# Kernel tuning notes

Hardware: AMD Instinct MI355X
Metric: run time of the kernel (lower is better)

Reference implementation:

```python
import jax, jax.numpy as jnp
import numpy as np

B, T, D, H = 4, 2048, 1024, 4
DK = D // H      # head_k_dim = 256
DV = D // H      # head_v_dim = 256
M = DK           # num_slots defaults to head_k_dim
GATE_NORM = 16.0
CLAMP_MIN, CLAMP_MAX = -32.0, 32.0
EPS = 1e-5
ROPE_BASE = 10000.0


def setup_inputs() -> dict:
    key = jax.random.key(0)
    ks = jax.random.split(key, 8)
    sd = 0.02  # stands in for xavier_uniform with gain 2**-2.5
    return {
        "hidden_states": jax.random.normal(ks[0], (B, T, D), jnp.float32),
        "q_w": jax.random.normal(ks[1], (D, D), jnp.float32) * sd,
        "k_w": jax.random.normal(ks[2], (D, D), jnp.float32) * sd,
        "v_w": jax.random.normal(ks[3], (D, D), jnp.float32) * sd,
        "g_w": jax.random.normal(ks[4], (D, D), jnp.float32) * sd,
        "s_w": jax.random.normal(ks[5], (D, H * M), jnp.float32) * sd,
        "sg_w": jax.random.normal(ks[6], (D, H), jnp.float32) * sd,
        "gn_w": jnp.ones((DV,), jnp.float32),
        "o_w": jax.random.normal(ks[7], (D, D), jnp.float32) * sd,
    }


def _rope(x):
    # x: [B, T, H, DK]; non-interleaved (flash-attn style) rotary, full head dim
    half = x.shape[-1] // 2
    inv = 1.0 / (ROPE_BASE ** (jnp.arange(half, dtype=jnp.float32) / half))
    ang = jnp.arange(x.shape[1], dtype=jnp.float32)[:, None] * inv[None, :]  # [T, half]
    cos = jnp.cos(ang)[None, :, None, :]
    sin = jnp.sin(ang)[None, :, None, :]
    x1, x2 = x[..., :half], x[..., half:]
    return jnp.concatenate([x1 * cos - x2 * sin, x2 * cos + x1 * sin], -1)


def _abc(q, k, v, s):
    # ABC linear attention with slot memory (fla chunk_abc semantics, g=None path).
    # q, k: [B,H,T,DK]; v: [B,H,T,DV]; s: [B,H,T,M] (clamped slot logits)
    scale = q.shape[-1] ** -0.5
    z = jax.lax.cumlogsumexp(s, axis=2)                    # running log-normalizer
    s_n = jnp.exp(s - z)                                   # normalized slot write weights
    g = jnp.exp(jnp.concatenate([z[:, :, :1], z[:, :, :-1]], 2) - z)  # per-step decay in (0,1]

    tm = lambda x: jnp.moveaxis(x, 2, 0)                   # time-major for scan

    # stage 1: key memory  hk[B,H,DK,M];  ok_t = scale * q_t @ hk_t
    def step_k(hk, inp):
        q_t, k_t, s_t, g_t = inp
        hk = hk * g_t[:, :, None, :] + k_t[..., None] * s_t[:, :, None, :]
        return hk, jnp.einsum('bhk,bhkm->bhm', q_t, hk)
    hk0 = jnp.zeros(q.shape[:2] + (q.shape[-1], s.shape[-1]), q.dtype)
    _, ok = jax.lax.scan(step_k, hk0, (tm(q * scale), tm(k), tm(s_n), tm(g)))

    qv = jax.nn.softmax(ok, axis=-1)                       # slot read weights, [T,B,H,M]

    # stage 2: value memory  hv[B,H,M,DV];  ov_t = qv_t @ hv_t
    def step_v(hv, inp):
        qv_t, v_t, s_t, g_t = inp
        hv = hv * g_t[..., None] + s_t[..., None] * v_t[:, :, None, :]
        return hv, jnp.einsum('bhm,bhmv->bhv', qv_t, hv)
    hv0 = jnp.zeros(v.shape[:2] + (s.shape[-1], v.shape[-1]), v.dtype)
    _, ov = jax.lax.scan(step_v, hv0, (qv, tm(v), tm(s_n), tm(g)))
    return jnp.moveaxis(ov, 0, 2)                          # [B,H,T,DV]


def reference(hidden_states, q_w, k_w, v_w, g_w, s_w, sg_w, gn_w, o_w):
    x = hidden_states
    q = (x @ q_w).reshape(B, T, H, DK)
    k = (x @ k_w).reshape(B, T, H, DK)
    v = (x @ v_w).reshape(B, T, H, DV).transpose(0, 2, 1, 3)       # [B,H,T,DV]
    q, k = _rope(q), _rope(k)
    q = q.transpose(0, 2, 1, 3)                                    # [B,H,T,DK]
    k = k.transpose(0, 2, 1, 3)

    s = (x @ s_w).reshape(B, T, H, M).transpose(0, 2, 1, 3)        # [B,H,T,M]
    s = jnp.clip(s, CLAMP_MIN, CLAMP_MAX)

    sg = jax.nn.log_sigmoid(x @ sg_w).transpose(0, 2, 1) / GATE_NORM  # [B,H,T]
    k = k * jnp.exp(jnp.cumsum(sg, axis=2))[..., None]

    o = _abc(q, k, v, s).transpose(0, 2, 1, 3)                     # [B,T,H,DV]

    g = (x @ g_w).reshape(B, T, H, DV)
    rms = o * jax.lax.rsqrt(jnp.mean(o * o, axis=-1, keepdims=True) + EPS) * gn_w
    o = (rms * g * jax.nn.sigmoid(g)).reshape(B, T, D)             # RMSNorm + swish gate
    return o @ o_w
```

## Files before the change

kernel.cpp:

```cpp
#include <hip/hip_runtime.h>
#include <hip/hip_bf16.h>
#include <stdint.h>
#include <stddef.h>
#include <math.h>

typedef __bf16 bf8_t __attribute__((ext_vector_type(8)));
typedef float  f4_t  __attribute__((ext_vector_type(4)));
typedef unsigned int u32;

#define DEV static __device__ __forceinline__

namespace abc {
constexpr int B = 4, T = 2048, D = 1024, H = 4;
constexpr int BT = B * T;
constexpr int CH = 64;
constexpr int NC = T / CH;
constexpr int BH = B * H;
constexpr float SCALE = 0.0625f;
constexpr float GN = 16.0f;
constexpr float EPS = 1e-5f;
}

DEV f4_t mfma16(bf8_t a, bf8_t b, f4_t c) {
  return __builtin_amdgcn_mfma_f32_16x16x32_bf16(a, b, c, 0, 0, 0);
}

DEV void glds16(const void* g, void* l) {
  __builtin_amdgcn_global_load_lds(
      (const __attribute__((address_space(1))) u32*)g,
      (__attribute__((address_space(3))) u32*)l, 16, 0, 0);
}

DEV __bf16* slice_addr(__bf16* base, int row, int cg ) {
  return base + (((cg >> 2) * 2 + (row >> 7)) * 4096
               + ((((row & 127) << 2) | ((cg & 3) ^ (row & 3))) * 8));
}
DEV const __bf16* slice_addr(const __bf16* base, int row, int cg) {
  return base + (((cg >> 2) * 2 + (row >> 7)) * 4096
               + ((((row & 127) << 2) | ((cg & 3) ^ (row & 3))) * 8));
}

DEV void stage_g(const __bf16* __restrict__ g, int S, __bf16* lds, int tid) {
  int m = tid >> 2;
  int q = (tid & 3) ^ ((m >> 1) & 3);
  glds16(g + (size_t)m * S + q * 8, lds + (tid & ~63) * 8);
}
DEV bf8_t bfrag_g(const __bf16* sl, int m, int quad) {
  return *reinterpret_cast<const bf8_t*>(sl + m * 32 + (((quad ^ (m >> 1)) & 3) << 3));
}

__global__ __launch_bounds__(256)
void cvt_x_kernel(const float* __restrict__ x, __bf16* __restrict__ xb)
{
  const int idx = blockIdx.x * 256 + threadIdx.x;
  const float4* src = reinterpret_cast<const float4*>(x);
  float4 a = src[(size_t)idx * 2];
  float4 b = src[(size_t)idx * 2 + 1];
  bf8_t o;
  o[0] = (__bf16)a.x; o[1] = (__bf16)a.y; o[2] = (__bf16)a.z; o[3] = (__bf16)a.w;
  o[4] = (__bf16)b.x; o[5] = (__bf16)b.y; o[6] = (__bf16)b.z; o[7] = (__bf16)b.w;
  reinterpret_cast<bf8_t*>(xb)[idx] = o;
}

__global__ __launch_bounds__(256)
void cvt_w_kernel(const float* __restrict__ w0, const float* __restrict__ w1,
                  const float* __restrict__ w2, const float* __restrict__ w3,
                  const float* __restrict__ w4, const float* __restrict__ w5,
                  __bf16* __restrict__ wt)
{
  const int z = blockIdx.z;
  const float* W = (z == 0) ? w0 : (z == 1) ? w1 : (z == 2) ? w2
                 : (z == 3) ? w3 : (z == 4) ? w4 : w5;
  const int n0 = blockIdx.x * 64, k0 = blockIdx.y * 64;
  __shared__ __bf16 Ts[64][72];
  const int tid = threadIdx.x;
  #pragma unroll
  for (int i = 0; i < 4; i++) {
    int p = tid + 256 * i;
    int row = p >> 4, c4 = p & 15;
    float4 v = *reinterpret_cast<const float4*>(W + (size_t)(k0 + row) * 1024 + n0 + c4 * 4);
    Ts[c4 * 4 + 0][row] = (__bf16)v.x;
    Ts[c4 * 4 + 1][row] = (__bf16)v.y;
    Ts[c4 * 4 + 2][row] = (__bf16)v.z;
    Ts[c4 * 4 + 3][row] = (__bf16)v.w;
  }
  __syncthreads();
  #pragma unroll
  for (int i = 0; i < 2; i++) {
    int p = tid + 256 * i;
    int n = p >> 3, kq = p & 7;
    bf8_t o = *reinterpret_cast<const bf8_t*>(&Ts[n][kq * 8]);
    *reinterpret_cast<bf8_t*>(wt + (size_t)z * 1024 * 1024 + (size_t)(n0 + n) * 1024 + k0 + kq * 8) = o;
  }
}

template<bool OUT_BF16, int NZ>
__global__ __launch_bounds__(512, 2)
void gemm256_kernel(const __bf16* __restrict__ A, const __bf16* __restrict__ BtB,
                    void* __restrict__ Cp)
{
  using namespace abc;
  constexpr int K = 1024;
  constexpr int NZT = 4 * NZ;
  const int bflat = blockIdx.x;
  const int xcd = bflat & 7;
  const int j = bflat >> 3;
  const int m_local = j / NZT;
  const int nz = j % NZT;
  const int nt = nz & 3, z = nz >> 2;
  const int m0 = (xcd * 4 + m_local) * 256;
  const int n0 = nt * 256;
  const __bf16* Bt = BtB + (size_t)z * K * 1024;

  __shared__ __bf16 LA[2][4][4096];
  __shared__ __bf16 LB[2][4][4096];

  const int tid = threadIdx.x;
  const int lane = tid & 63, wv = tid >> 6;
  const int wr = wv >> 2, wc = wv & 3;
  const int quad = lane >> 4, l16 = lane & 15;
  const f4_t fzero = {0.f, 0.f, 0.f, 0.f};
  f4_t acc[8][4];
  #pragma unroll
  for (int fr = 0; fr < 8; fr++)
    #pragma unroll
    for (int fc = 0; fc < 4; fc++) acc[fr][fc] = fzero;

  auto issue4 = [&](int kt, int ks) {
    const int db = kt & 1;
    const int kcol = kt * 64 + ks * 32;
    stage_g(A  + (size_t)(m0 +   0) * K + kcol, K, &LA[db][0 + ks][0], tid);
    stage_g(A  + (size_t)(m0 + 128) * K + kcol, K, &LA[db][2 + ks][0], tid);
    stage_g(Bt + (size_t)(n0 +   0) * K + kcol, K, &LB[db][0 + ks][0], tid);
    stage_g(Bt + (size_t)(n0 + 128) * K + kcol, K, &LB[db][2 + ks][0], tid);
  };

  issue4(0, 0); issue4(0, 1);

  for (int kt = 0; kt < 16; kt++) {
    const int db = kt & 1;
    const bool last = (kt == 15);
    #pragma unroll
    for (int ks = 0; ks < 2; ks++) {
      if (last && ks == 1) asm volatile("s_waitcnt vmcnt(0)\ns_barrier" ::: "memory");
      else                 asm volatile("s_waitcnt vmcnt(4)\ns_barrier" ::: "memory");
      bf8_t af[8], bfv[4];
      #pragma unroll
      for (int fr = 0; fr < 8; fr++)
        af[fr] = bfrag_g(&LA[db][wr * 2 + ks][0], fr * 16 + l16, quad);
      #pragma unroll
      for (int fc = 0; fc < 4; fc++)
        bfv[fc] = bfrag_g(&LB[db][(wc >> 1) * 2 + ks][0], (wc & 1) * 64 + fc * 16 + l16, quad);
      if (!last) issue4(kt + 1, ks);
      __builtin_amdgcn_s_setprio(1);
      #pragma unroll
      for (int fr = 0; fr < 8; fr++)
        #pragma unroll
        for (int fc = 0; fc < 4; fc++)
          acc[fr][fc] = mfma16(af[fr], bfv[fc], acc[fr][fc]);
      __builtin_amdgcn_s_setprio(0);
    }
  }

  const int crow = m0 + wr * 128, ccol = n0 + wc * 64;
  if (OUT_BF16) {
    __bf16* C = (__bf16*)Cp + (size_t)z * BT * 1024;
    #pragma unroll
    for (int fr = 0; fr < 8; fr++)
      #pragma unroll
      for (int fc = 0; fc < 4; fc++)
        #pragma unroll
        for (int r = 0; r < 4; r++)
          C[(size_t)(crow + fr * 16 + quad * 4 + r) * 1024 + ccol + fc * 16 + l16] =
              (__bf16)acc[fr][fc][r];
  } else {
    float* C = (float*)Cp;
    #pragma unroll
    for (int fr = 0; fr < 8; fr++)
      #pragma unroll
      for (int fc = 0; fc < 4; fc++)
        #pragma unroll
        for (int r = 0; r < 4; r++)
          C[(size_t)(crow + fr * 16 + quad * 4 + r) * 1024 + ccol + fc * 16 + l16] =
              acc[fr][fc][r];
  }
}

__global__ __launch_bounds__(256)
void sg_kernel(const float* __restrict__ x, const float* __restrict__ sgw,
               float* __restrict__ sgl)
{
  using namespace abc;
  const int wvid = threadIdx.x >> 6, lane = threadIdx.x & 63;
  const int bt = blockIdx.x * 4 + wvid;
  const float* xr = x + (size_t)bt * 1024;
  float a0 = 0, a1 = 0, a2 = 0, a3 = 0;
  #pragma unroll 4
  for (int u = 0; u < 16; u++) {
    int i = u * 64 + lane;
    float xv = xr[i];
    float4 w = *reinterpret_cast<const float4*>(sgw + (size_t)i * 4);
    a0 += xv * w.x; a1 += xv * w.y; a2 += xv * w.z; a3 += xv * w.w;
  }
  #pragma unroll
  for (int off = 32; off > 0; off >>= 1) {
    a0 += __shfl_down(a0, off);
    a1 += __shfl_down(a1, off);
    a2 += __shfl_down(a2, off);
    a3 += __shfl_down(a3, off);
  }
  if (lane == 0) {
    const int b = bt >> 11, t = bt & (T - 1);
    float r[4] = {a0, a1, a2, a3};
    #pragma unroll
    for (int h = 0; h < 4; h++) {
      float v = r[h];
      float ls = fminf(v, 0.f) - log1pf(expf(-fabsf(v)));
      sgl[(size_t)(b * 4 + h) * T + t] = ls * (1.0f / GN);
    }
  }
}

__global__ __launch_bounds__(256)
void scan_kernel(const float* __restrict__ sgl, float* __restrict__ sgc)
{
  using namespace abc;
  const int bh = blockIdx.x;
  const float* in = sgl + (size_t)bh * T;
  float* out = sgc + (size_t)bh * T;
  __shared__ float part[256];
  const int tid = threadIdx.x;
  float v[8]; float s = 0.f;
  #pragma unroll
  for (int i = 0; i < 8; i++) { v[i] = in[tid * 8 + i]; s += v[i]; }
  part[tid] = s;
  __syncthreads();
  for (int off = 1; off < 256; off <<= 1) {
    float a = (tid >= off) ? part[tid - off] : 0.f;
    __syncthreads();
    part[tid] += a;
    __syncthreads();
  }
  float run = (tid > 0) ? part[tid - 1] : 0.f;
  #pragma unroll
  for (int i = 0; i < 8; i++) { run += v[i]; out[tid * 8 + i] = run; }
}

__global__ __launch_bounds__(256)
void prep_kernel(__bf16* __restrict__ q, __bf16* __restrict__ k,
                 __bf16* __restrict__ s, const float* __restrict__ sgc)
{
  using namespace abc;
  const int bt = blockIdx.x;
  const int b = bt >> 11, t = bt & (T - 1);
  const int tid = threadIdx.x;
  const size_t ro = (size_t)bt * 1024;
  #pragma unroll
  for (int i = 0; i < 2; i++) {
    int p = tid + 256 * i;
    int h = p >> 7, d = p & 127;
    float inv = expf(-(float)d * (9.210340371976184f / 128.0f));
    float ang = (float)t * inv;
    float sn, cs;
    sincosf(ang, &sn, &cs);
    size_t base = ro + (size_t)h * 256 + d;
    float q1 = (float)q[base], q2 = (float)q[base + 128];
    q[base]       = (__bf16)(q1 * cs - q2 * sn);
    q[base + 128] = (__bf16)(q2 * cs + q1 * sn);
    float dec = expf(sgc[(size_t)(b * 4 + h) * T + t]);
    float k1 = (float)k[base], k2 = (float)k[base + 128];
    k[base]       = (__bf16)((k1 * cs - k2 * sn) * dec);
    k[base + 128] = (__bf16)((k2 * cs + k1 * sn) * dec);
  }
  #pragma unroll
  for (int i = 0; i < 4; i++) {
    int e = tid + 256 * i;
    float v = (float)s[ro + e];
    v = fminf(fmaxf(v, -32.f), 32.f);
    s[ro + e] = (__bf16)expf(v);
  }
}

template<bool NEW0, bool NEW1>
__global__ __launch_bounds__(256)
void transpose_kernel(const __bf16* __restrict__ s0, const __bf16* __restrict__ s1,
                      __bf16* __restrict__ d0, __bf16* __restrict__ d1)
{
  using namespace abc;
  const int c = blockIdx.x, bh = blockIdx.y, z = blockIdx.z;
  const int b = bh >> 2, h = bh & 3;
  const size_t R = (size_t)b * T + (size_t)c * CH;
  const int F = h * 256;
  const __bf16* src = z ? s1 : s0;
  __bf16* dst = (z ? d1 : d0) + ((size_t)bh * NC + c) * (256 * 64);
  const bool NEWL = z ? NEW1 : NEW0;
  __shared__ __bf16 L[256 * 64];
  const int tid = threadIdx.x;
  #pragma unroll
  for (int j = 0; j < 8; j++) {
    int p = tid + 256 * j;
    int t = p >> 5, fc = p & 31;
    bf8_t v = *reinterpret_cast<const bf8_t*>(src + (R + t) * 1024 + F + fc * 8);
    const int sw = ((t >> 3) ^ (fc & 7)) * 8 + (t & 7);
    #pragma unroll
    for (int u = 0; u < 8; u++)
      L[(fc * 8 + u) * 64 + sw] = v[u];
  }
  __syncthreads();
  #pragma unroll
  for (int j = 0; j < 8; j++) {
    int p = tid + 256 * j;
    int f = p >> 3, q = p & 7;
    int phys = q ^ ((f >> 3) & 7);
    bf8_t o = *reinterpret_cast<const bf8_t*>(&L[f * 64 + phys * 8]);
    __bf16* daddr = NEWL ? slice_addr(dst, f, q)
                         : dst + (size_t)f * 64 + q * 8;
    *reinterpret_cast<bf8_t*>(daddr) = o;
  }
}

__global__ __launch_bounds__(256)
void chunkstate_kernel(const __bf16* __restrict__ KT, const __bf16* __restrict__ VT,
                       const __bf16* __restrict__ AT,
                       __bf16* __restrict__ HKc, __bf16* __restrict__ HVc,
                       float* __restrict__ csA)
{
  using namespace abc;
  const int c = blockIdx.x, bh = blockIdx.y, part = blockIdx.z;
  const size_t TB = ((size_t)bh * NC + c) * (256 * 64);
  const bool isHV = part >= 2;
  const int p2 = part & 1;
  const __bf16* Aop = (isHV ? VT : AT) + TB;
  const __bf16* Bop = (isHV ? AT : KT) + TB;
  const int tid = threadIdx.x;
  if (part == 2) {
    float ssum = 0.f;
    #pragma unroll
    for (int u = 0; u < 8; u++) {
      bf8_t v = *reinterpret_cast<const bf8_t*>(slice_addr(AT + TB, tid, u));
      #pragma unroll
      for (int w = 0; w < 8; w++) ssum += (float)v[w];
    }
    csA[((size_t)bh * NC + c) * 256 + tid] = ssum;
  }
  const int lane = tid & 63, wvid = tid >> 6;
  const int quad = lane >> 4, l16 = lane & 15;
  const int row0 = p2 * 128 + wvid * 32;
  const f4_t fzero = {0.f, 0.f, 0.f, 0.f};
  f4_t acc[2][16];
  #pragma unroll
  for (int a = 0; a < 2; a++)
    #pragma unroll
    for (int ct = 0; ct < 16; ct++) acc[a][ct] = fzero;
  #pragma unroll
  for (int ks = 0; ks < 2; ks++) {
    const int cg = ks * 4 + quad;
    bf8_t af0 = *reinterpret_cast<const bf8_t*>(slice_addr(Aop, row0 + l16, cg));
    bf8_t af1 = *reinterpret_cast<const bf8_t*>(slice_addr(Aop, row0 + 16 + l16, cg));
    #pragma unroll
    for (int ct = 0; ct < 16; ct++) {
      bf8_t bv;
      if (isHV)
        bv = *reinterpret_cast<const bf8_t*>(slice_addr(Bop, ct * 16 + l16, cg));
      else
        bv = *reinterpret_cast<const bf8_t*>(Bop + (size_t)(ct * 16 + l16) * 64 + ks * 32 + quad * 8);
      acc[0][ct] = mfma16(af0, bv, acc[0][ct]);
      acc[1][ct] = mfma16(af1, bv, acc[1][ct]);
    }
  }
  __bf16* out = (isHV ? HVc : HKc) + ((size_t)bh * NC + c) * 65536;
  #pragma unroll
  for (int rt = 0; rt < 2; rt++)
    #pragma unroll
    for (int ct = 0; ct < 16; ct++)
      #pragma unroll
      for (int r = 0; r < 4; r++) {
        const int mg = row0 + rt * 16 + quad * 4 + r;
        const int n  = ct * 16 + l16;
        *(slice_addr(out, mg, n >> 3) + (n & 7)) = (__bf16)acc[rt][ct][r];
      }
}

__global__ __launch_bounds__(256)
void prefix_state_kernel(__bf16* __restrict__ HKc, __bf16* __restrict__ HVc)
{
  using namespace abc;
  const int bh = blockIdx.y;
  __bf16* base = (blockIdx.z ? HVc : HKc) + (size_t)bh * NC * 65536;
  const int e = (blockIdx.x * 256 + threadIdx.x) * 8;
  float run[8];
  #pragma unroll
  for (int u = 0; u < 8; u++) run[u] = 0.f;
  #pragma unroll 4
  for (int c = 0; c < NC; c++) {
    __bf16* p = base + (size_t)c * 65536 + e;
    bf8_t v = *reinterpret_cast<const bf8_t*>(p);
    bf8_t o;
    #pragma unroll
    for (int u = 0; u < 8; u++) { o[u] = (__bf16)run[u]; run[u] += (float)v[u]; }
    *reinterpret_cast<bf8_t*>(p) = o;
  }
}

__global__ __launch_bounds__(256)
void prefix_csa_kernel(float* __restrict__ csA)
{
  using namespace abc;
  const int bh = blockIdx.x, m = threadIdx.x;
  float run = 0.f;
  for (int c = 0; c < NC; c++) {
    float* p = csA + ((size_t)bh * NC + c) * 256 + m;
    float v = *p; *p = run; run += v;
  }
}

__global__ __launch_bounds__(256)
void attn_kernel(const __bf16* __restrict__ qg, const __bf16* __restrict__ kg,
                 const __bf16* __restrict__ ag, const __bf16* __restrict__ gg,
                 const __bf16* __restrict__ ATp, const __bf16* __restrict__ VTp,
                 const __bf16* __restrict__ HKp, const __bf16* __restrict__ HVp,
                 const float* __restrict__ Zp, const float* __restrict__ gnw,
                 __bf16* __restrict__ yout)
{
  using namespace abc;
  const int c = blockIdx.x, bh = blockIdx.y;
  const int b = bh >> 2, h = bh & 3;
  const size_t R = (size_t)b * T + (size_t)c * CH;
  const int F = h * 256;
  const int tid = threadIdx.x;
  const int lane = tid & 63, wvid = tid >> 6;
  const int quad = lane >> 4, l16 = lane & 15;

  __shared__ __bf16 Ws[64][264];
  __shared__ __bf16 S1s[64][72];
  __shared__ float zs[256];
  __shared__ float gns[256];

  const __bf16* atb = ATp + ((size_t)bh * NC + c) * (256 * 64);
  const __bf16* vtb = VTp + ((size_t)bh * NC + c) * (256 * 64);
  const __bf16* hkb = HKp + ((size_t)bh * NC + c) * 65536;
  const __bf16* hvb = HVp + ((size_t)bh * NC + c) * 65536;
  const __bf16* kbase = kg + R * 1024 + F;
  const __bf16* abase = ag + R * 1024 + F;

  zs[tid] = Zp[((size_t)bh * NC + c) * 256 + tid];
  gns[tid] = gnw[tid];
  __syncthreads();

  const int lsw = l16 * 32 + ((quad ^ (l16 & 3)) << 3);
  const int rowoff = l16 * 1024 + quad * 8;

  const __bf16* qrow = qg + (R + wvid * 16 + l16) * 1024 + F;
  bf8_t aq[8];
  #pragma unroll
  for (int ks = 0; ks < 8; ks++)
    aq[ks] = *reinterpret_cast<const bf8_t*>(qrow + ks * 32 + quad * 8);

  const f4_t fzero = {0.f, 0.f, 0.f, 0.f};

  f4_t s1a[4];
  #pragma unroll
  for (int it = 0; it < 4; it++) s1a[it] = fzero;
  #pragma unroll
  for (int ks = 0; ks < 8; ks++) {
    #pragma unroll
    for (int it = 0; it < 4; it++) {
      bf8_t bk = *reinterpret_cast<const bf8_t*>(kbase + it * 16 * 1024 + rowoff + ks * 32);
      s1a[it] = mfma16(aq[ks], bk, s1a[it]);
    }
  }
  #pragma unroll
  for (int it = 0; it < 4; it++)
    #pragma unroll
    for (int r = 0; r < 4; r++) {
      int tl = wvid * 16 + quad * 4 + r;
      int il = it * 16 + l16;
      S1s[tl][il] = (il <= tl) ? (__bf16)s1a[it][r] : (__bf16)0.0f;
    }

  f4_t aok[16], acum[16];
  #pragma unroll
  for (int mt = 0; mt < 16; mt++) { aok[mt] = fzero; acum[mt] = fzero; }
  #pragma unroll
  for (int iks = 0; iks < 2; iks++) {
    bf8_t s1f = *reinterpret_cast<const bf8_t*>(&S1s[wvid * 16 + l16][iks * 32 + quad * 8]);
    bf8_t lf;
    #pragma unroll
    for (int u = 0; u < 8; u++)
      lf[u] = (iks * 32 + quad * 8 + u <= wvid * 16 + l16) ? (__bf16)1.0f : (__bf16)0.0f;
    #pragma unroll
    for (int rh = 0; rh < 2; rh++) {
      #pragma unroll
      for (int m8 = 0; m8 < 8; m8++) {
        bf8_t bfa = *reinterpret_cast<const bf8_t*>(atb + (iks * 2 + rh) * 4096 + m8 * 512 + lsw);
        aok[rh * 8 + m8]  = mfma16(s1f, bfa, aok[rh * 8 + m8]);
        acum[rh * 8 + m8] = mfma16(lf,  bfa, acum[rh * 8 + m8]);
      }
    }
  }

  #pragma unroll
  for (int ks = 0; ks < 8; ks++) {
    #pragma unroll
    for (int rh = 0; rh < 2; rh++) {
      #pragma unroll
      for (int m8 = 0; m8 < 8; m8++) {
        bf8_t bv = *reinterpret_cast<const bf8_t*>(hkb + (ks * 2 + rh) * 4096 + m8 * 512 + lsw);
        aok[rh * 8 + m8] = mfma16(aq[ks], bv, aok[rh * 8 + m8]);
      }
    }
  }

  #pragma unroll
  for (int r = 0; r < 4; r++) {
    float ovv[16], sa[16];
    float mx = -3.0e38f;
    #pragma unroll
    for (int mt = 0; mt < 16; mt++) {
      sa[mt] = zs[mt * 16 + l16] + acum[mt][r];
      ovv[mt] = SCALE * aok[mt][r] / sa[mt];
      mx = fmaxf(mx, ovv[mt]);
    }
    #pragma unroll
    for (int off = 1; off < 16; off <<= 1) mx = fmaxf(mx, __shfl_xor(mx, off));
    float se = 0.f;
    #pragma unroll
    for (int mt = 0; mt < 16; mt++) { ovv[mt] = __expf(ovv[mt] - mx); se += ovv[mt]; }
    #pragma unroll
    for (int off = 1; off < 16; off <<= 1) se += __shfl_xor(se, off);
    float inv = 1.0f / se;
    int tl = wvid * 16 + quad * 4 + r;
    #pragma unroll
    for (int mt = 0; mt < 16; mt++)
      Ws[tl][mt * 16 + l16] = (__bf16)(ovv[mt] * inv / sa[mt]);
  }

  f4_t pacc[4];
  #pragma unroll
  for (int it = 0; it < 4; it++) pacc[it] = fzero;
  #pragma unroll
  for (int ks = 0; ks < 8; ks++) {
    bf8_t wf = *reinterpret_cast<const bf8_t*>(&Ws[wvid * 16 + l16][ks * 32 + quad * 8]);
    #pragma unroll
    for (int it = 0; it < 4; it++) {
      bf8_t ba = *reinterpret_cast<const bf8_t*>(abase + it * 16 * 1024 + rowoff + ks * 32);
      pacc[it] = mfma16(wf, ba, pacc[it]);
    }
  }
  #pragma unroll
  for (int it = 0; it < 4; it++)
    #pragma unroll
    for (int r = 0; r < 4; r++) {
      int tl = wvid * 16 + quad * 4 + r;
      int il = it * 16 + l16;
      S1s[tl][il] = (il <= tl) ? (__bf16)pacc[it][r] : (__bf16)0.0f;
    }

  f4_t oacc[16];
  #pragma unroll
  for (int vt = 0; vt < 16; vt++) oacc[vt] = fzero;
  #pragma unroll
  for (int ks = 0; ks < 8; ks++) {
    bf8_t wf = *reinterpret_cast<const bf8_t*>(&Ws[wvid * 16 + l16][ks * 32 + quad * 8]);
    #pragma unroll
    for (int rh = 0; rh < 2; rh++) {
      #pragma unroll
      for (int v8 = 0; v8 < 8; v8++) {
        bf8_t bv = *reinterpret_cast<const bf8_t*>(hvb + (ks * 2 + rh) * 4096 + v8 * 512 + lsw);
        oacc[rh * 8 + v8] = mfma16(wf, bv, oacc[rh * 8 + v8]);
      }
    }
  }

  #pragma unroll
  for (int iks = 0; iks < 2; iks++) {
    bf8_t pf = *reinterpret_cast<const bf8_t*>(&S1s[wvid * 16 + l16][iks * 32 + quad * 8]);
    #pragma unroll
    for (int rh = 0; rh < 2; rh++) {
      #pragma unroll
      for (int v8 = 0; v8 < 8; v8++) {
        bf8_t bvt = *reinterpret_cast<const bf8_t*>(vtb + (iks * 2 + rh) * 4096 + v8 * 512 + lsw);
        oacc[rh * 8 + v8] = mfma16(pf, bvt, oacc[rh * 8 + v8]);
      }
    }
  }

  #pragma unroll
  for (int r = 0; r < 4; r++) {
    float ss = 0.f;
    #pragma unroll
    for (int vt = 0; vt < 16; vt++) ss += oacc[vt][r] * oacc[vt][r];
    #pragma unroll
    for (int off = 1; off < 16; off <<= 1) ss += __shfl_xor(ss, off);
    float rinv = rsqrtf(ss * (1.0f / 256.0f) + EPS);
    int tl = wvid * 16 + quad * 4 + r;
    const __bf16* grow = gg + (R + tl) * 1024 + F;
    __bf16* yrow = yout + (R + tl) * 1024 + F;
    #pragma unroll
    for (int vt = 0; vt < 16; vt++) {
      int v = vt * 16 + l16;
      float gvl = (float)grow[v];
      float yv = oacc[vt][r] * rinv * gns[v] * gvl / (1.0f + __expf(-gvl));
      yrow[v] = (__bf16)yv;
    }
  }
}

extern "C" void kernel_launch(void* const* d_in, const int* in_sizes, int n_in,
                              void* d_out, int out_size, void* d_ws, size_t ws_size,
                              hipStream_t stream) {
  using namespace abc;
  (void)in_sizes; (void)n_in; (void)out_size; (void)ws_size;
  const float* x    = (const float*)d_in[0];
  const float* q_w  = (const float*)d_in[1];
  const float* k_w  = (const float*)d_in[2];
  const float* v_w  = (const float*)d_in[3];
  const float* g_w  = (const float*)d_in[4];
  const float* s_w  = (const float*)d_in[5];
  const float* sg_w = (const float*)d_in[6];
  const float* gn_w = (const float*)d_in[7];
  const float* o_w  = (const float*)d_in[8];
  float* out = (float*)d_out;

  char* ws = (char*)d_ws;
  const size_t PROJ = (size_t)BT * 1024;
  __bf16* proj = (__bf16*)ws;
  __bf16* q_bf = proj + 0 * PROJ;
  __bf16* k_bf = proj + 1 * PROJ;
  __bf16* v_bf = proj + 2 * PROJ;
  __bf16* g_bf = proj + 3 * PROJ;
  __bf16* a_bf = proj + 4 * PROJ;
  __bf16* xb   = proj + 5 * PROJ;
  float* sgl = (float*)(ws + (size_t)96 * 1024 * 1024);
  float* sgc = sgl + (size_t)BH * T;
  float* csA = sgc + (size_t)BH * T;
  __bf16* HKc = (__bf16*)(ws + (size_t)97 * 1024 * 1024);
  __bf16* HVc = HKc + (size_t)BH * NC * 65536;
  __bf16* wt  = (__bf16*)(ws + (size_t)225 * 1024 * 1024);
  __bf16* KT  = (__bf16*)(ws + (size_t)237 * 1024 * 1024);
  __bf16* VT  = xb;
  __bf16* AT  = v_bf;
  __bf16* y_bf = KT;

  dim3 blk(256);
  dim3 blk512(512);
  cvt_w_kernel<<<dim3(16, 16, 6), blk, 0, stream>>>(q_w, k_w, v_w, g_w, s_w, o_w, wt);
  cvt_x_kernel<<<dim3(BT * 1024 / (256 * 8)), blk, 0, stream>>>(x, xb);
  gemm256_kernel<true, 5><<<dim3(32 * 4 * 5), blk512, 0, stream>>>(xb, wt, proj);
  sg_kernel<<<dim3(BT / 4), blk, 0, stream>>>(x, sg_w, sgl);
  scan_kernel<<<dim3(BH), blk, 0, stream>>>(sgl, sgc);
  prep_kernel<<<dim3(BT), blk, 0, stream>>>(q_bf, k_bf, a_bf, sgc);
  transpose_kernel<false, true><<<dim3(NC, BH, 2), blk, 0, stream>>>(k_bf, v_bf, KT, VT);
  transpose_kernel<true, true><<<dim3(NC, BH, 1), blk, 0, stream>>>(a_bf, a_bf, AT, AT);
  chunkstate_kernel<<<dim3(NC, BH, 4), blk, 0, stream>>>(KT, VT, AT, HKc, HVc, csA);
  prefix_state_kernel<<<dim3(32, BH, 2), blk, 0, stream>>>(HKc, HVc);
  prefix_csa_kernel<<<dim3(BH), blk, 0, stream>>>(csA);
  attn_kernel<<<dim3(NC, BH), blk, 0, stream>>>(
      q_bf, k_bf, a_bf, g_bf, AT, VT, HKc, HVc, csA, gn_w, y_bf);
  gemm256_kernel<false, 1><<<dim3(32 * 4), blk512, 0, stream>>>(
      y_bf, wt + (size_t)5 * 1024 * 1024, out);
}
```

Baseline: 473.9 us.

## Pre-tile GEMM operands into swizzled slice layout for contiguous LDS staging

The producers of the GEMM operands (x conversion, weight transpose, and the gated-norm output) now write bf16 data directly in a pre-swizzled 128-row by 32-column slice layout. The GEMM stage then copies each 4096-element slice to LDS with fully contiguous 16-byte global_load_lds transactions instead of strided row gathers. This is meant to cut address computation and improve global load coalescing in the GEMM main loop. The cost is scattered element-wise stores in the epilogue of the attention kernel, and every consumer of these buffers must agree on the layout.

```diff
diff --git a/kernel.cpp b/kernel.cpp
--- a/kernel.cpp
+++ b/kernel.cpp
@@ -40,26 +40,32 @@
                + ((((row & 127) << 2) | ((cg & 3) ^ (row & 3))) * 8));
 }
 
-DEV void stage_g(const __bf16* __restrict__ g, int S, __bf16* lds, int tid) {
-  int m = tid >> 2;
-  int q = (tid & 3) ^ ((m >> 1) & 3);
-  glds16(g + (size_t)m * S + q * 8, lds + (tid & ~63) * 8);
+DEV __bf16* gslice_addr(__bf16* base, int row, int col) {
+  return base + ((size_t)((row >> 7) * 32 + (col >> 5)) * 4096
+       + ((((row & 127) << 2) | (((col >> 3) & 3) ^ ((row >> 1) & 3))) * 8)
+       + (col & 7));
+}
+DEV const __bf16* gslice_addr(const __bf16* base, int row, int col) {
+  return base + ((size_t)((row >> 7) * 32 + (col >> 5)) * 4096
+       + ((((row & 127) << 2) | (((col >> 3) & 3) ^ ((row >> 1) & 3))) * 8)
+       + (col & 7));
 }
 DEV bf8_t bfrag_g(const __bf16* sl, int m, int quad) {
   return *reinterpret_cast<const bf8_t*>(sl + m * 32 + (((quad ^ (m >> 1)) & 3) << 3));
 }
 
 __global__ __launch_bounds__(256)
-void cvt_x_kernel(const float* __restrict__ x, __bf16* __restrict__ xb)
+void cvt_x_kernel(const float* __restrict__ x, __bf16* __restrict__ xs)
 {
   const int idx = blockIdx.x * 256 + threadIdx.x;
+  const int row = idx >> 7, c8 = idx & 127;
   const float4* src = reinterpret_cast<const float4*>(x);
   float4 a = src[(size_t)idx * 2];
   float4 b = src[(size_t)idx * 2 + 1];
   bf8_t o;
   o[0] = (__bf16)a.x; o[1] = (__bf16)a.y; o[2] = (__bf16)a.z; o[3] = (__bf16)a.w;
   o[4] = (__bf16)b.x; o[5] = (__bf16)b.y; o[6] = (__bf16)b.z; o[7] = (__bf16)b.w;
-  reinterpret_cast<bf8_t*>(xb)[idx] = o;
+  *reinterpret_cast<bf8_t*>(gslice_addr(xs, row, c8 * 8)) = o;
 }
 
 __global__ __launch_bounds__(256)
@@ -90,7 +96,8 @@
     int p = tid + 256 * i;
     int n = p >> 3, kq = p & 7;
     bf8_t o = *reinterpret_cast<const bf8_t*>(&Ts[n][kq * 8]);
-    *reinterpret_cast<bf8_t*>(wt + (size_t)z * 1024 * 1024 + (size_t)(n0 + n) * 1024 + k0 + kq * 8) = o;
+    *reinterpret_cast<bf8_t*>(
+        gslice_addr(wt + (size_t)z * 1024 * 1024, n0 + n, k0 + kq * 8)) = o;
   }
 }
 
@@ -128,11 +135,16 @@
 
   auto issue4 = [&](int kt, int ks) {
     const int db = kt & 1;
-    const int kcol = kt * 64 + ks * 32;
-    stage_g(A  + (size_t)(m0 +   0) * K + kcol, K, &LA[db][0 + ks][0], tid);
-    stage_g(A  + (size_t)(m0 + 128) * K + kcol, K, &LA[db][2 + ks][0], tid);
-    stage_g(Bt + (size_t)(n0 +   0) * K + kcol, K, &LB[db][0 + ks][0], tid);
-    stage_g(Bt + (size_t)(n0 + 128) * K + kcol, K, &LB[db][2 + ks][0], tid);
+    const int kc = kt * 2 + ks;
+    const __bf16* a0 = A  + (size_t)(((m0 >> 7) + 0) * 32 + kc) * 4096;
+    const __bf16* a1 = A  + (size_t)(((m0 >> 7) + 1) * 32 + kc) * 4096;
+    const __bf16* b0 = Bt + (size_t)(((n0 >> 7) + 0) * 32 + kc) * 4096;
+    const __bf16* b1 = Bt + (size_t)(((n0 >> 7) + 1) * 32 + kc) * 4096;
+    const int ldst = (tid & ~63) * 8;
+    glds16(a0 + (size_t)tid * 8, &LA[db][0 + ks][ldst]);
+    glds16(a1 + (size_t)tid * 8, &LA[db][2 + ks][ldst]);
+    glds16(b0 + (size_t)tid * 8, &LB[db][0 + ks][ldst]);
+    glds16(b1 + (size_t)tid * 8, &LB[db][2 + ks][ldst]);
   };
 
   issue4(0, 0); issue4(0, 1);
@@ -595,13 +607,12 @@
     float rinv = rsqrtf(ss * (1.0f / 256.0f) + EPS);
     int tl = wvid * 16 + quad * 4 + r;
     const __bf16* grow = gg + (R + tl) * 1024 + F;
-    __bf16* yrow = yout + (R + tl) * 1024 + F;
     #pragma unroll
     for (int vt = 0; vt < 16; vt++) {
       int v = vt * 16 + l16;
       float gvl = (float)grow[v];
       float yv = oacc[vt][r] * rinv * gns[v] * gvl / (1.0f + __expf(-gvl));
-      yrow[v] = (__bf16)yv;
+      *gslice_addr(yout, (int)(R + tl), F + v) = (__bf16)yv;
     }
   }
 }
```

Result: no change. 472.7 us (median of 2 runs) (-0.3%).
